# Performance work log

Measured on AMD Instinct MI355X. Metric: run time of the kernel, lower is better.

## Reference

```python
import jax, jax.numpy as jnp
import numpy as np

DIM = 768
HEADS = 12
HEAD_DIM = DIM // HEADS
HIDDEN = 4 * DIM
SCALE = HEAD_DIM ** -0.5
LN_EPS = 1e-5


def layer_norm(x, g, b):
    mu = jnp.mean(x, axis=-1, keepdims=True)
    var = jnp.var(x, axis=-1, keepdims=True)
    return (x - mu) * jax.lax.rsqrt(var + LN_EPS) * g + b


def setup_inputs() -> dict:
    key = jax.random.key(0)
    ks = jax.random.split(key, 10)
    B, N = 2, 2048
    s = 0.02
    return {
        "x": jax.random.normal(ks[0], (B, N, DIM), jnp.float32),
        "elevation": jax.random.uniform(ks[1], (B, N), jnp.float32),
        "qkv_w": jax.random.normal(ks[2], (DIM, 3 * DIM), jnp.float32) * s,
        "qkv_b": jnp.zeros((3 * DIM,), jnp.float32),
        "proj_w": jax.random.normal(ks[3], (DIM, DIM), jnp.float32) * s,
        "proj_b": jnp.zeros((DIM,), jnp.float32),
        "ln1_g": jnp.ones((DIM,), jnp.float32),
        "ln1_b": jnp.zeros((DIM,), jnp.float32),
        "ln2_g": jnp.ones((DIM,), jnp.float32),
        "ln2_b": jnp.zeros((DIM,), jnp.float32),
        "fc1_w": jax.random.normal(ks[4], (DIM, HIDDEN), jnp.float32) * s,
        "fc1_b": jnp.zeros((HIDDEN,), jnp.float32),
        "fc2_w": jax.random.normal(ks[5], (HIDDEN, DIM), jnp.float32) * s,
        "fc2_b": jnp.zeros((DIM,), jnp.float32),
        "barrier": jnp.asarray(3.0, jnp.float32),
    }


def reference(x, elevation, qkv_w, qkv_b, proj_w, proj_b, ln1_g, ln1_b,
              ln2_g, ln2_b, fc1_w, fc1_b, fc2_w, fc2_b, barrier):
    B, N, C = x.shape
    h = layer_norm(x, ln1_g, ln1_b)
    qkv = (h @ qkv_w + qkv_b).reshape(B, N, 3, HEADS, HEAD_DIM)
    q, k, v = jnp.moveaxis(qkv, 2, 0)  # each [B, N, H, D]
    # scores: [B, H, N, N]
    scores = jnp.einsum('bnhd,bmhd->bhnm', q, k) * SCALE
    w = jax.nn.softmax(scores, axis=-1)
    # pairwise elevation mask [B, N, N]: sigmoid(-s * (elev_j - elev_i))
    diff = elevation[:, None, :] - elevation[:, :, None]
    mask = jnp.clip(jax.nn.sigmoid(-barrier * diff), 1e-6, 1.0)
    w = w * mask[:, None, :, :]
    w = w / (jnp.sum(w, axis=-1, keepdims=True) + 1e-8)
    attn_out = jnp.einsum('bhnm,bmhd->bnhd', w, v).reshape(B, N, C)
    x = x + attn_out @ proj_w + proj_b
    h2 = layer_norm(x, ln2_g, ln2_b)
    mlp = jax.nn.gelu(h2 @ fc1_w + fc1_b, approximate=False) @ fc2_w + fc2_b
    return x + mlp
```

## Files before the change

kernel.cpp:

```cpp
#include <hip/hip_runtime.h>
#include <math.h>

#define DIM 768
#define HEADS 12
#define SEQ 2048
#define ROWS 4096
#define LN_EPS 1e-5f

typedef __attribute__((ext_vector_type(8))) short short8;
typedef __attribute__((ext_vector_type(4))) float floatx4;
typedef unsigned short ushort_t;

__device__ __forceinline__ ushort_t f2bf(float x) {
    unsigned u = __float_as_uint(x);
    u += 0x7fff + ((u >> 16) & 1);
    return (ushort_t)(u >> 16);
}

__device__ __forceinline__ void gload_lds16(const void* g, void* l) {
    __builtin_amdgcn_global_load_lds((const __attribute__((address_space(1))) void*)g,
                                     (__attribute__((address_space(3))) void*)l, 16, 0, 0);
}

__launch_bounds__(256)
__global__ void wconv_kernel(const float* __restrict__ W, ushort_t* __restrict__ WT,
                             int K, int N) {
    __shared__ __align__(16) ushort_t s[64][72];
    int k0 = blockIdx.y * 64, n0 = blockIdx.x * 64;
    int t = threadIdx.x;
    int rr0 = t >> 4, c4 = (t & 15) * 4;
    for (int rr = rr0; rr < 64; rr += 16) {
        float4 w = *(const float4*)(W + (size_t)(k0 + rr) * N + n0 + c4);
        s[c4 + 0][rr] = f2bf(w.x); s[c4 + 1][rr] = f2bf(w.y);
        s[c4 + 2][rr] = f2bf(w.z); s[c4 + 3][rr] = f2bf(w.w);
    }
    __syncthreads();
    int nl = t >> 2, kq = (t & 3) * 16;
    uint4 a = *(const uint4*)&s[nl][kq];
    uint4 b = *(const uint4*)&s[nl][kq + 8];
    *(uint4*)(WT + (size_t)(n0 + nl) * K + k0 + kq) = a;
    *(uint4*)(WT + (size_t)(n0 + nl) * K + k0 + kq + 8) = b;
}

__launch_bounds__(256)
__global__ void gelev_kernel(const float* __restrict__ elev, const float* __restrict__ barrier_p,
                             float* __restrict__ G, float* __restrict__ iG,
                             float* __restrict__ C2) {
    int i = blockIdx.x * 256 + threadIdx.x;
    float be = barrier_p[0] * elev[i];
    G[i]  = __expf(be);
    iG[i] = __expf(-be);
    C2[i] = be;
}

__launch_bounds__(256)
__global__ void ln_kernel(const float* __restrict__ x, const float* __restrict__ g,
                          const float* __restrict__ b, ushort_t* __restrict__ out) {
    int row = blockIdx.x;
    const float* xr = x + (size_t)row * DIM;
    int t = threadIdx.x;
    float v0 = xr[t], v1 = xr[t + 256], v2 = xr[t + 512];
    float s  = v0 + v1 + v2;
    float ss = v0 * v0 + v1 * v1 + v2 * v2;
    #pragma unroll
    for (int o = 32; o >= 1; o >>= 1) { s += __shfl_xor(s, o); ss += __shfl_xor(ss, o); }
    __shared__ float rs[4], rss[4];
    int wid = t >> 6, lane = t & 63;
    if (lane == 0) { rs[wid] = s; rss[wid] = ss; }
    __syncthreads();
    if (t == 0) {
        float S = 0.f, SS = 0.f;
        for (int i = 0; i < 4; i++) { S += rs[i]; SS += rss[i]; }
        rs[0] = S; rss[0] = SS;
    }
    __syncthreads();
    float mean = rs[0] * (1.0f / DIM);
    float var  = rss[0] * (1.0f / DIM) - mean * mean;
    float rstd = rsqrtf(var + LN_EPS);
    ushort_t* orow = out + (size_t)row * DIM;
    orow[t]       = f2bf((v0 - mean) * rstd * g[t]       + b[t]);
    orow[t + 256] = f2bf((v1 - mean) * rstd * g[t + 256] + b[t + 256]);
    orow[t + 512] = f2bf((v2 - mean) * rstd * g[t + 512] + b[t + 512]);
}

template<int BN, int EPI>
__launch_bounds__(256)
__global__ void gemm_bf16(const ushort_t* __restrict__ A, const ushort_t* __restrict__ WT,
                          const float* __restrict__ bias, const float* __restrict__ res,
                          float* __restrict__ outF, ushort_t* __restrict__ outB,
                          ushort_t* __restrict__ qb, ushort_t* __restrict__ kb,
                          ushort_t* __restrict__ vb, int N, int K) {
    constexpr int NT = BN / 32;
    __shared__ __align__(16) ushort_t sA[64 * 32];
    __shared__ __align__(16) ushort_t sB[BN * 32];
    int t = threadIdx.x;
    int row0 = blockIdx.y * 64, col0 = blockIdx.x * BN;
    int wid = t >> 6, lane = t & 63;
    int wm = wid >> 1, wn = wid & 1;
    int cl = lane & 15, quad = lane >> 4;

    floatx4 acc[2][NT];
    #pragma unroll
    for (int i = 0; i < 2; i++)
        #pragma unroll
        for (int j = 0; j < NT; j++) { floatx4 z = {0.f, 0.f, 0.f, 0.f}; acc[i][j] = z; }

    for (int k0 = 0; k0 < K; k0 += 32) {
        {
            int r = t >> 2, sub = t & 3;
            gload_lds16(A + (size_t)(row0 + r) * K + k0 + sub * 8, &sA[t * 8]);
        }
        #pragma unroll
        for (int i = 0; i < BN / 64; i++) {
            int c = i * 256 + t;
            int r = c >> 2, sub = c & 3;
            gload_lds16(WT + (size_t)(col0 + r) * K + k0 + sub * 8, &sB[c * 8]);
        }
        __syncthreads();
        short8 a[2], b[NT];
        #pragma unroll
        for (int i = 0; i < 2; i++)
            a[i] = *(const short8*)&sA[(wm * 32 + i * 16 + cl) * 32 + quad * 8];
        #pragma unroll
        for (int j = 0; j < NT; j++)
            b[j] = *(const short8*)&sB[(wn * (BN / 2) + j * 16 + cl) * 32 + quad * 8];
        #pragma unroll
        for (int i = 0; i < 2; i++)
            #pragma unroll
            for (int j = 0; j < NT; j++)
                acc[i][j] = __builtin_amdgcn_mfma_f32_16x16x32_bf16(a[i], b[j], acc[i][j], 0, 0, 0);
        __syncthreads();
    }

    #pragma unroll
    for (int i = 0; i < 2; i++) {
        #pragma unroll
        for (int j = 0; j < NT; j++) {
            int gcol = col0 + wn * (BN / 2) + j * 16 + cl;
            float bv = bias[gcol];
            #pragma unroll
            for (int rg = 0; rg < 4; rg++) {
                int grow = row0 + wm * 32 + i * 16 + quad * 4 + rg;
                float v = acc[i][j][rg] + bv;
                if (EPI == 0) {
                    int which = gcol / 768;
                    int hc = gcol - which * 768;
                    int h = hc >> 6, d = hc & 63;
                    int b_ = grow >> 11, n = grow & 2047;
                    size_t bh = (size_t)(b_ * 12 + h);
                    if (which == 0)      qb[(bh * 2048 + n) * 64 + d] = f2bf(v * 0.125f);
                    else if (which == 1) kb[(bh * 2048 + n) * 64 + d] = f2bf(v);
                    else                 vb[(bh * 64 + d) * 2048 + n] = f2bf(v);
                } else if (EPI == 1) {
                    v = 0.5f * v * (1.f + erff(v * 0.70710678118654752f));
                    outB[(size_t)grow * N + gcol] = f2bf(v);
                } else {
                    v += res[(size_t)grow * N + gcol];
                    outF[(size_t)grow * N + gcol] = v;
                }
            }
        }
    }
}

__launch_bounds__(256)
__global__ void attn_mfma(const ushort_t* __restrict__ qb, const ushort_t* __restrict__ kb,
                          const ushort_t* __restrict__ vb, const float* __restrict__ G,
                          const float* __restrict__ iG, const float* __restrict__ C2,
                          ushort_t* __restrict__ attn) {
    __shared__ __align__(16) ushort_t Qs[64 * 64];
    __shared__ __align__(16) ushort_t Ks[2][64 * 64];
    __shared__ __align__(16) ushort_t Vt[2][64 * 64];
    __shared__ __align__(16) ushort_t Ps[64 * 64];
    __shared__ float Gjs[2][64];
    int qt = blockIdx.x, h = blockIdx.y, b = blockIdx.z;
    int t = threadIdx.x, wid = t >> 6, lane = t & 63;
    int cl = lane & 15, quad = lane >> 4;
    int q0 = qt * 64;
    size_t bh = (size_t)(b * 12 + h);

    const ushort_t* qbase = qb + (bh * 2048 + q0) * 64;
    #pragma unroll
    for (int i = 0; i < 2; i++) {
        int c = i * 256 + t, row = c >> 3, blk = c & 7;
        gload_lds16(qbase + (row << 6) + ((blk ^ (row & 7)) << 3), &Qs[c * 8]);
    }
    int qrow = b * 2048 + q0 + wid * 16 + quad * 4;
    float4 g4  = *(const float4*)(G  + qrow);
    float4 ig4 = *(const float4*)(iG + qrow);
    float4 c24 = *(const float4*)(C2 + qrow);
    float gi[4]  = {g4.x, g4.y, g4.z, g4.w};
    float igi[4] = {ig4.x, ig4.y, ig4.z, ig4.w};
    floatx4 c2init = {c24.x, c24.y, c24.z, c24.w};

    {
        const ushort_t* kbase = kb + bh * 2048 * 64;
        const ushort_t* vbase = vb + bh * 131072;
        #pragma unroll
        for (int i = 0; i < 2; i++) {
            int c = i * 256 + t, row = c >> 3, blk = c & 7;
            gload_lds16(kbase + (row << 6) + ((blk ^ (row & 7)) << 3), &Ks[0][c * 8]);
            gload_lds16(vbase + (size_t)row * 2048 + ((blk ^ (row & 7)) << 3), &Vt[0][c * 8]);
        }
        if (t < 64) Gjs[0][t] = G[b * 2048 + t];
    }

    floatx4 o[4];
    #pragma unroll
    for (int j = 0; j < 4; j++) { floatx4 z = {0.f, 0.f, 0.f, 0.f}; o[j] = z; }
    float se[4] = {0.f, 0.f, 0.f, 0.f}, sem[4] = {0.f, 0.f, 0.f, 0.f};

    for (int kt = 0; kt < 32; kt++) {
        int cur = kt & 1;
        __syncthreads();
        if (kt < 31) {
            int k0n = (kt + 1) * 64;
            const ushort_t* kbase = kb + (bh * 2048 + k0n) * 64;
            const ushort_t* vbase = vb + bh * 131072 + k0n;
            #pragma unroll
            for (int i = 0; i < 2; i++) {
                int c = i * 256 + t, row = c >> 3, blk = c & 7;
                gload_lds16(kbase + (row << 6) + ((blk ^ (row & 7)) << 3), &Ks[cur ^ 1][c * 8]);
                gload_lds16(vbase + (size_t)row * 2048 + ((blk ^ (row & 7)) << 3), &Vt[cur ^ 1][c * 8]);
            }
            if (t < 64) Gjs[cur ^ 1][t] = G[b * 2048 + k0n + t];
        }

        float gjv[4];
        #pragma unroll
        for (int nt = 0; nt < 4; nt++) gjv[nt] = Gjs[cur][nt * 16 + cl];

        floatx4 s[4];
        #pragma unroll
        for (int nt = 0; nt < 4; nt++) s[nt] = c2init;
        #pragma unroll
        for (int kh = 0; kh < 2; kh++) {
            short8 aq = *(const short8*)&Qs[((wid * 16 + cl) << 6) + (((kh * 4 + quad) ^ (cl & 7)) << 3)];
            #pragma unroll
            for (int nt = 0; nt < 4; nt++) {
                short8 bk = *(const short8*)&Ks[cur][((nt * 16 + cl) << 6) + (((kh * 4 + quad) ^ (cl & 7)) << 3)];
                s[nt] = __builtin_amdgcn_mfma_f32_16x16x32_bf16(aq, bk, s[nt], 0, 0, 0);
            }
        }

        #pragma unroll
        for (int rg = 0; rg < 4; rg++) {
            int prow = wid * 16 + quad * 4 + rg;
            int r8 = prow & 7, pbase = prow << 6, csub = cl & 7, chi = cl >> 3;
            #pragma unroll
            for (int nt = 0; nt < 4; nt++) {
                float tf = __expf(s[nt][rg]);
                float R  = __builtin_amdgcn_rcpf(gi[rg] + gjv[nt]);
                float p  = tf * R;
                se[rg]  += tf;
                sem[rg] += p;
                Ps[pbase + (((nt * 2 + chi) ^ r8) << 3) + csub] = (ushort_t)(__float_as_uint(p) >> 16);
            }
        }

        #pragma unroll
        for (int kh = 0; kh < 2; kh++) {
            short8 ap = *(const short8*)&Ps[((wid * 16 + cl) << 6) + (((kh * 4 + quad) ^ (cl & 7)) << 3)];
            #pragma unroll
            for (int dt = 0; dt < 4; dt++) {
                short8 bv = *(const short8*)&Vt[cur][((dt * 16 + cl) << 6) + (((kh * 4 + quad) ^ (cl & 7)) << 3)];
                o[dt] = __builtin_amdgcn_mfma_f32_16x16x32_bf16(ap, bv, o[dt], 0, 0, 0);
            }
        }
    }

    #pragma unroll
    for (int rg = 0; rg < 4; rg++) {
        float a = se[rg], m = sem[rg];
        #pragma unroll
        for (int off = 1; off < 16; off <<= 1) { a += __shfl_xor(a, off); m += __shfl_xor(m, off); }
        float inv = __builtin_amdgcn_rcpf(m + 1e-8f * a * igi[rg]);
        int grow = b * 2048 + q0 + wid * 16 + quad * 4 + rg;
        #pragma unroll
        for (int dt = 0; dt < 4; dt++)
            attn[(size_t)grow * 768 + h * 64 + dt * 16 + cl] = f2bf(o[dt][rg] * inv);
    }
}

extern "C" void kernel_launch(void* const* d_in, const int* in_sizes, int n_in,
                              void* d_out, int out_size, void* d_ws, size_t ws_size,
                              hipStream_t stream) {
    const float* x      = (const float*)d_in[0];
    const float* elev   = (const float*)d_in[1];
    const float* qkv_w  = (const float*)d_in[2];
    const float* qkv_b  = (const float*)d_in[3];
    const float* proj_w = (const float*)d_in[4];
    const float* proj_b = (const float*)d_in[5];
    const float* ln1_g  = (const float*)d_in[6];
    const float* ln1_b  = (const float*)d_in[7];
    const float* ln2_g  = (const float*)d_in[8];
    const float* ln2_b  = (const float*)d_in[9];
    const float* fc1_w  = (const float*)d_in[10];
    const float* fc1_b  = (const float*)d_in[11];
    const float* fc2_w  = (const float*)d_in[12];
    const float* fc2_b  = (const float*)d_in[13];
    const float* barrier= (const float*)d_in[14];
    float* out = (float*)d_out;
    char* ws = (char*)d_ws;

    ushort_t* h    = (ushort_t*)(ws + 0);
    ushort_t* qb   = (ushort_t*)(ws + 6291456);
    ushort_t* kb   = (ushort_t*)(ws + 12582912);
    ushort_t* vb   = (ushort_t*)(ws + 18874368);
    ushort_t* f1   = (ushort_t*)(ws + 0);
    ushort_t* attn = (ushort_t*)(ws + 25165824);
    ushort_t* h2   = (ushort_t*)(ws + 31457280);
    float*    Gf   = (float*)(ws + 31457280);
    float*    iGf  = (float*)(ws + 31473664);
    float*    C2f  = (float*)(ws + 31490048);
    ushort_t* qkvT = (ushort_t*)(ws + 37748736);
    ushort_t* projT= (ushort_t*)(ws + 41287680);
    ushort_t* fc1T = (ushort_t*)(ws + 42467328);
    ushort_t* fc2T = (ushort_t*)(ws + 47185920);

    wconv_kernel<<<dim3(2304 / 64, 768 / 64),  256, 0, stream>>>(qkv_w, qkvT, 768, 2304);
    wconv_kernel<<<dim3(768 / 64,  768 / 64),  256, 0, stream>>>(proj_w, projT, 768, 768);
    wconv_kernel<<<dim3(3072 / 64, 768 / 64),  256, 0, stream>>>(fc1_w, fc1T, 768, 3072);
    wconv_kernel<<<dim3(768 / 64,  3072 / 64), 256, 0, stream>>>(fc2_w, fc2T, 3072, 768);
    gelev_kernel<<<16, 256, 0, stream>>>(elev, barrier, Gf, iGf, C2f);

    ln_kernel<<<ROWS, 256, 0, stream>>>(x, ln1_g, ln1_b, h);
    gemm_bf16<128, 0><<<dim3(2304 / 128, 64), 256, 0, stream>>>(
        h, qkvT, qkv_b, nullptr, nullptr, nullptr, qb, kb, vb, 2304, 768);
    attn_mfma<<<dim3(32, HEADS, 2), 256, 0, stream>>>(qb, kb, vb, Gf, iGf, C2f, attn);
    gemm_bf16<64, 2><<<dim3(768 / 64, 64), 256, 0, stream>>>(
        attn, projT, proj_b, x, out, nullptr, nullptr, nullptr, nullptr, 768, 768);
    ln_kernel<<<ROWS, 256, 0, stream>>>(out, ln2_g, ln2_b, h2);
    gemm_bf16<128, 1><<<dim3(3072 / 128, 64), 256, 0, stream>>>(
        h2, fc1T, fc1_b, nullptr, nullptr, f1, nullptr, nullptr, nullptr, 3072, 768);
    gemm_bf16<64, 2><<<dim3(768 / 64, 64), 256, 0, stream>>>(
        f1, fc2T, fc2_b, out, out, nullptr, nullptr, nullptr, nullptr, 768, 3072);
}
```

Before: 352.9 us.

## Switch attention and QKV/FC1 GEMMs to 32x32 MFMA tiles, merge weight conversions

Adds a 128x128-tile GEMM built on 32x32x16 bf16 MFMA for the QKV and FC1 projections. The attention kernel is rewritten the same way: each wave computes a 32x32 score tile, and the two key-half partial outputs are combined through LDS. Output rows are then staged in LDS and written with coalesced 16-byte stores. The four weight conversion launches are merged into one kernel, and the iG array and the 1e-8 epsilon term in the normaliser are dropped. The aim is fewer MFMA instructions per flop, more data reuse and less launch overhead, at the cost of more registers per thread and an extra LDS reduction and barriers in attention.

```diff
diff --git a/kernel.cpp b/kernel.cpp
--- a/kernel.cpp
+++ b/kernel.cpp
@@ -9,6 +9,7 @@
 
 typedef __attribute__((ext_vector_type(8))) short short8;
 typedef __attribute__((ext_vector_type(4))) float floatx4;
+typedef __attribute__((ext_vector_type(16))) float floatx16;
 typedef unsigned short ushort_t;
 
 __device__ __forceinline__ ushort_t f2bf(float x) {
@@ -23,10 +24,19 @@
 }
 
 __launch_bounds__(256)
-__global__ void wconv_kernel(const float* __restrict__ W, ushort_t* __restrict__ WT,
-                             int K, int N) {
+__global__ void wconv_all(const float* __restrict__ w0, const float* __restrict__ w1,
+                          const float* __restrict__ w2, const float* __restrict__ w3,
+                          ushort_t* __restrict__ t0, ushort_t* __restrict__ t1,
+                          ushort_t* __restrict__ t2, ushort_t* __restrict__ t3) {
     __shared__ __align__(16) ushort_t s[64][72];
-    int k0 = blockIdx.y * 64, n0 = blockIdx.x * 64;
+    int bid = blockIdx.x;
+    const float* W; ushort_t* WT; int K, N, nx, id;
+    if (bid < 432)       { W = w0; WT = t0; K = 768;  N = 2304; nx = 36; id = bid; }
+    else if (bid < 576)  { W = w1; WT = t1; K = 768;  N = 768;  nx = 12; id = bid - 432; }
+    else if (bid < 1152) { W = w2; WT = t2; K = 768;  N = 3072; nx = 48; id = bid - 576; }
+    else                 { W = w3; WT = t3; K = 3072; N = 768;  nx = 12; id = bid - 1152; }
+    int tx = id % nx, ty = id / nx;
+    int k0 = ty * 64, n0 = tx * 64;
     int t = threadIdx.x;
     int rr0 = t >> 4, c4 = (t & 15) * 4;
     for (int rr = rr0; rr < 64; rr += 16) {
@@ -44,12 +54,10 @@
 
 __launch_bounds__(256)
 __global__ void gelev_kernel(const float* __restrict__ elev, const float* __restrict__ barrier_p,
-                             float* __restrict__ G, float* __restrict__ iG,
-                             float* __restrict__ C2) {
+                             float* __restrict__ G, float* __restrict__ C2) {
     int i = blockIdx.x * 256 + threadIdx.x;
     float be = barrier_p[0] * elev[i];
     G[i]  = __expf(be);
-    iG[i] = __expf(-be);
     C2[i] = be;
 }
 
@@ -83,13 +91,91 @@
     orow[t + 512] = f2bf((v2 - mean) * rstd * g[t + 512] + b[t + 512]);
 }
 
+template<int EPI>
+__launch_bounds__(256)
+__global__ void gemm32(const ushort_t* __restrict__ A, const ushort_t* __restrict__ WT,
+                       const float* __restrict__ bias, ushort_t* __restrict__ outB,
+                       ushort_t* __restrict__ qb, ushort_t* __restrict__ kb,
+                       ushort_t* __restrict__ vb, int N, int K) {
+    __shared__ __align__(16) ushort_t sA[128 * 32];
+    __shared__ __align__(16) ushort_t sB[128 * 32];
+    int t = threadIdx.x;
+    int row0 = blockIdx.y * 128, col0 = blockIdx.x * 128;
+    int wid = t >> 6, lane = t & 63, l31 = lane & 31, hb = lane >> 5;
+    int wm = wid >> 1, wn = wid & 1;
+
+    floatx16 acc[2][2];
+    #pragma unroll
+    for (int i = 0; i < 2; i++)
+        #pragma unroll
+        for (int j = 0; j < 2; j++)
+            #pragma unroll
+            for (int e = 0; e < 16; e++) acc[i][j][e] = 0.f;
+
+    for (int k0 = 0; k0 < K; k0 += 32) {
+        #pragma unroll
+        for (int i = 0; i < 2; i++) {
+            int c = i * 256 + t;
+            int r = c >> 2, blk = c & 3;
+            gload_lds16(A  + (size_t)(row0 + r) * K + k0 + ((blk ^ (r & 3)) << 3), &sA[c * 8]);
+            gload_lds16(WT + (size_t)(col0 + r) * K + k0 + ((blk ^ (r & 3)) << 3), &sB[c * 8]);
+        }
+        __syncthreads();
+        #pragma unroll
+        for (int s = 0; s < 2; s++) {
+            int blk = s * 2 + hb;
+            int ra0 = wm * 64 + l31, ra1 = ra0 + 32;
+            int rb0 = wn * 64 + l31, rb1 = rb0 + 32;
+            short8 a0 = *(const short8*)&sA[ra0 * 32 + ((blk ^ (ra0 & 3)) << 3)];
+            short8 a1 = *(const short8*)&sA[ra1 * 32 + ((blk ^ (ra1 & 3)) << 3)];
+            short8 b0 = *(const short8*)&sB[rb0 * 32 + ((blk ^ (rb0 & 3)) << 3)];
+            short8 b1 = *(const short8*)&sB[rb1 * 32 + ((blk ^ (rb1 & 3)) << 3)];
+            acc[0][0] = __builtin_amdgcn_mfma_f32_32x32x16_bf16(a0, b0, acc[0][0], 0, 0, 0);
+            acc[0][1] = __builtin_amdgcn_mfma_f32_32x32x16_bf16(a0, b1, acc[0][1], 0, 0, 0);
+            acc[1][0] = __builtin_amdgcn_mfma_f32_32x32x16_bf16(a1, b0, acc[1][0], 0, 0, 0);
+            acc[1][1] = __builtin_amdgcn_mfma_f32_32x32x16_bf16(a1, b1, acc[1][1], 0, 0, 0);
+        }
+        __syncthreads();
+    }
+
+    #pragma unroll
+    for (int mt = 0; mt < 2; mt++) {
+        #pragma unroll
+        for (int nt = 0; nt < 2; nt++) {
+            int gcol = col0 + wn * 64 + nt * 32 + l31;
+            float bv = bias[gcol];
+            if (EPI == 0) {
+                int which = gcol / 768;
+                int hc = gcol - which * 768;
+                int hh = hc >> 6, d = hc & 63;
+                #pragma unroll
+                for (int rg = 0; rg < 16; rg++) {
+                    int grow = row0 + wm * 64 + mt * 32 + (rg & 3) + 8 * (rg >> 2) + 4 * hb;
+                    float v = acc[mt][nt][rg] + bv;
+                    int b_ = grow >> 11, n = grow & 2047;
+                    size_t bhh = (size_t)(b_ * 12 + hh);
+                    if (which == 0)      qb[(bhh * 2048 + n) * 64 + d] = f2bf(v * 0.125f);
+                    else if (which == 1) kb[(bhh * 2048 + n) * 64 + d] = f2bf(v);
+                    else                 vb[(bhh * 64 + d) * 2048 + n] = f2bf(v);
+                }
+            } else {
+                #pragma unroll
+                for (int rg = 0; rg < 16; rg++) {
+                    int grow = row0 + wm * 64 + mt * 32 + (rg & 3) + 8 * (rg >> 2) + 4 * hb;
+                    float v = acc[mt][nt][rg] + bv;
+                    v = 0.5f * v * (1.f + erff(v * 0.70710678118654752f));
+                    outB[(size_t)grow * N + gcol] = f2bf(v);
+                }
+            }
+        }
+    }
+}
+
 template<int BN, int EPI>
 __launch_bounds__(256)
 __global__ void gemm_bf16(const ushort_t* __restrict__ A, const ushort_t* __restrict__ WT,
                           const float* __restrict__ bias, const float* __restrict__ res,
-                          float* __restrict__ outF, ushort_t* __restrict__ outB,
-                          ushort_t* __restrict__ qb, ushort_t* __restrict__ kb,
-                          ushort_t* __restrict__ vb, int N, int K) {
+                          float* __restrict__ outF, int N, int K) {
     constexpr int NT = BN / 32;
     __shared__ __align__(16) ushort_t sA[64 * 32];
     __shared__ __align__(16) ushort_t sB[BN * 32];
@@ -141,23 +227,8 @@
             #pragma unroll
             for (int rg = 0; rg < 4; rg++) {
                 int grow = row0 + wm * 32 + i * 16 + quad * 4 + rg;
-                float v = acc[i][j][rg] + bv;
-                if (EPI == 0) {
-                    int which = gcol / 768;
-                    int hc = gcol - which * 768;
-                    int h = hc >> 6, d = hc & 63;
-                    int b_ = grow >> 11, n = grow & 2047;
-                    size_t bh = (size_t)(b_ * 12 + h);
-                    if (which == 0)      qb[(bh * 2048 + n) * 64 + d] = f2bf(v * 0.125f);
-                    else if (which == 1) kb[(bh * 2048 + n) * 64 + d] = f2bf(v);
-                    else                 vb[(bh * 64 + d) * 2048 + n] = f2bf(v);
-                } else if (EPI == 1) {
-                    v = 0.5f * v * (1.f + erff(v * 0.70710678118654752f));
-                    outB[(size_t)grow * N + gcol] = f2bf(v);
-                } else {
-                    v += res[(size_t)grow * N + gcol];
-                    outF[(size_t)grow * N + gcol] = v;
-                }
+                float v = acc[i][j][rg] + bv + res[(size_t)grow * N + gcol];
+                outF[(size_t)grow * N + gcol] = v;
             }
         }
     }
@@ -166,18 +237,17 @@
 __launch_bounds__(256)
 __global__ void attn_mfma(const ushort_t* __restrict__ qb, const ushort_t* __restrict__ kb,
                           const ushort_t* __restrict__ vb, const float* __restrict__ G,
-                          const float* __restrict__ iG, const float* __restrict__ C2,
-                          ushort_t* __restrict__ attn) {
-    __shared__ __align__(16) ushort_t Qs[64 * 64];
-    __shared__ __align__(16) ushort_t Ks[2][64 * 64];
-    __shared__ __align__(16) ushort_t Vt[2][64 * 64];
-    __shared__ __align__(16) ushort_t Ps[64 * 64];
-    __shared__ float Gjs[2][64];
-    int qt = blockIdx.x, h = blockIdx.y, b = blockIdx.z;
-    int t = threadIdx.x, wid = t >> 6, lane = t & 63;
-    int cl = lane & 15, quad = lane >> 4;
+                          const float* __restrict__ C2, ushort_t* __restrict__ attn) {
+    __shared__ __align__(16) ushort_t Qs[4096];
+    __shared__ __align__(16) ushort_t Ks[2][4096];
+    __shared__ __align__(16) ushort_t Vt[2][4096];
+    __shared__ __align__(16) ushort_t Ps[4096];
+    __shared__ float semL[2][64];
+    int qt = blockIdx.x, hh = blockIdx.y, b = blockIdx.z;
+    int t = threadIdx.x, wid = t >> 6, lane = t & 63, l31 = lane & 31, hb = lane >> 5;
+    int wm = wid >> 1, wn = wid & 1;
     int q0 = qt * 64;
-    size_t bh = (size_t)(b * 12 + h);
+    size_t bh = (size_t)(b * 12 + hh);
 
     const ushort_t* qbase = qb + (bh * 2048 + q0) * 64;
     #pragma unroll
@@ -185,13 +255,14 @@
         int c = i * 256 + t, row = c >> 3, blk = c & 7;
         gload_lds16(qbase + (row << 6) + ((blk ^ (row & 7)) << 3), &Qs[c * 8]);
     }
-    int qrow = b * 2048 + q0 + wid * 16 + quad * 4;
-    float4 g4  = *(const float4*)(G  + qrow);
-    float4 ig4 = *(const float4*)(iG + qrow);
-    float4 c24 = *(const float4*)(C2 + qrow);
-    float gi[4]  = {g4.x, g4.y, g4.z, g4.w};
-    float igi[4] = {ig4.x, ig4.y, ig4.z, ig4.w};
-    floatx4 c2init = {c24.x, c24.y, c24.z, c24.w};
+
+    float gi[16]; floatx16 c2v;
+    #pragma unroll
+    for (int rg = 0; rg < 16; rg++) {
+        int rr = (rg & 3) + 8 * (rg >> 2) + 4 * hb;
+        int gr = b * 2048 + q0 + wm * 32 + rr;
+        gi[rg] = G[gr]; c2v[rg] = C2[gr];
+    }
 
     {
         const ushort_t* kbase = kb + bh * 2048 * 64;
@@ -202,13 +273,14 @@
             gload_lds16(kbase + (row << 6) + ((blk ^ (row & 7)) << 3), &Ks[0][c * 8]);
             gload_lds16(vbase + (size_t)row * 2048 + ((blk ^ (row & 7)) << 3), &Vt[0][c * 8]);
         }
-        if (t < 64) Gjs[0][t] = G[b * 2048 + t];
-    }
-
-    floatx4 o[4];
-    #pragma unroll
-    for (int j = 0; j < 4; j++) { floatx4 z = {0.f, 0.f, 0.f, 0.f}; o[j] = z; }
-    float se[4] = {0.f, 0.f, 0.f, 0.f}, sem[4] = {0.f, 0.f, 0.f, 0.f};
+    }
+
+    floatx16 o0, o1;
+    float semP[16];
+    #pragma unroll
+    for (int e = 0; e < 16; e++) { o0[e] = 0.f; o1[e] = 0.f; semP[e] = 0.f; }
+
+    int arow = wm * 32 + l31, brow = wn * 32 + l31, x7 = l31 & 7;
 
     for (int kt = 0; kt < 32; kt++) {
         int cur = kt & 1;
@@ -223,63 +295,81 @@
                 gload_lds16(kbase + (row << 6) + ((blk ^ (row & 7)) << 3), &Ks[cur ^ 1][c * 8]);
                 gload_lds16(vbase + (size_t)row * 2048 + ((blk ^ (row & 7)) << 3), &Vt[cur ^ 1][c * 8]);
             }
-            if (t < 64) Gjs[cur ^ 1][t] = G[b * 2048 + k0n + t];
-        }
-
-        float gjv[4];
-        #pragma unroll
-        for (int nt = 0; nt < 4; nt++) gjv[nt] = Gjs[cur][nt * 16 + cl];
-
-        floatx4 s[4];
-        #pragma unroll
-        for (int nt = 0; nt < 4; nt++) s[nt] = c2init;
-        #pragma unroll
-        for (int kh = 0; kh < 2; kh++) {
-            short8 aq = *(const short8*)&Qs[((wid * 16 + cl) << 6) + (((kh * 4 + quad) ^ (cl & 7)) << 3)];
-            #pragma unroll
-            for (int nt = 0; nt < 4; nt++) {
-                short8 bk = *(const short8*)&Ks[cur][((nt * 16 + cl) << 6) + (((kh * 4 + quad) ^ (cl & 7)) << 3)];
-                s[nt] = __builtin_amdgcn_mfma_f32_16x16x32_bf16(aq, bk, s[nt], 0, 0, 0);
-            }
-        }
-
-        #pragma unroll
-        for (int rg = 0; rg < 4; rg++) {
-            int prow = wid * 16 + quad * 4 + rg;
-            int r8 = prow & 7, pbase = prow << 6, csub = cl & 7, chi = cl >> 3;
-            #pragma unroll
-            for (int nt = 0; nt < 4; nt++) {
-                float tf = __expf(s[nt][rg]);
-                float R  = __builtin_amdgcn_rcpf(gi[rg] + gjv[nt]);
-                float p  = tf * R;
-                se[rg]  += tf;
-                sem[rg] += p;
-                Ps[pbase + (((nt * 2 + chi) ^ r8) << 3) + csub] = (ushort_t)(__float_as_uint(p) >> 16);
-            }
-        }
-
-        #pragma unroll
-        for (int kh = 0; kh < 2; kh++) {
-            short8 ap = *(const short8*)&Ps[((wid * 16 + cl) << 6) + (((kh * 4 + quad) ^ (cl & 7)) << 3)];
-            #pragma unroll
-            for (int dt = 0; dt < 4; dt++) {
-                short8 bv = *(const short8*)&Vt[cur][((dt * 16 + cl) << 6) + (((kh * 4 + quad) ^ (cl & 7)) << 3)];
-                o[dt] = __builtin_amdgcn_mfma_f32_16x16x32_bf16(ap, bv, o[dt], 0, 0, 0);
-            }
-        }
-    }
-
-    #pragma unroll
-    for (int rg = 0; rg < 4; rg++) {
-        float a = se[rg], m = sem[rg];
-        #pragma unroll
-        for (int off = 1; off < 16; off <<= 1) { a += __shfl_xor(a, off); m += __shfl_xor(m, off); }
-        float inv = __builtin_amdgcn_rcpf(m + 1e-8f * a * igi[rg]);
-        int grow = b * 2048 + q0 + wid * 16 + quad * 4 + rg;
-        #pragma unroll
-        for (int dt = 0; dt < 4; dt++)
-            attn[(size_t)grow * 768 + h * 64 + dt * 16 + cl] = f2bf(o[dt][rg] * inv);
-    }
+        }
+        float gj = G[b * 2048 + kt * 64 + wn * 32 + l31];
+
+        floatx16 s = c2v;
+        #pragma unroll
+        for (int s4 = 0; s4 < 4; s4++) {
+            short8 aq = *(const short8*)&Qs[(arow << 6) + (((s4 * 2 + hb) ^ x7) << 3)];
+            short8 bk = *(const short8*)&Ks[cur][(brow << 6) + (((s4 * 2 + hb) ^ x7) << 3)];
+            s = __builtin_amdgcn_mfma_f32_32x32x16_bf16(aq, bk, s, 0, 0, 0);
+        }
+
+        #pragma unroll
+        for (int rg = 0; rg < 16; rg++) {
+            int rr = (rg & 3) + 8 * (rg >> 2) + 4 * hb;
+            int qrow = wm * 32 + rr;
+            float tf = __expf(s[rg]);
+            float p  = tf * __builtin_amdgcn_rcpf(gi[rg] + gj);
+            semP[rg] += p;
+            Ps[(qrow << 6) + (((wn * 4 + (l31 >> 3)) ^ (qrow & 7)) << 3) + (l31 & 7)] =
+                (ushort_t)(__float_as_uint(p) >> 16);
+        }
+
+        #pragma unroll
+        for (int s2 = 0; s2 < 2; s2++) {
+            int blk = wn * 4 + s2 * 2 + hb;
+            short8 ap  = *(const short8*)&Ps[(arow << 6) + ((blk ^ x7) << 3)];
+            short8 bv0 = *(const short8*)&Vt[cur][(l31 << 6) + ((blk ^ x7) << 3)];
+            short8 bv1 = *(const short8*)&Vt[cur][((32 + l31) << 6) + ((blk ^ x7) << 3)];
+            o0 = __builtin_amdgcn_mfma_f32_32x32x16_bf16(ap, bv0, o0, 0, 0, 0);
+            o1 = __builtin_amdgcn_mfma_f32_32x32x16_bf16(ap, bv1, o1, 0, 0, 0);
+        }
+    }
+
+    #pragma unroll
+    for (int rg = 0; rg < 16; rg++) {
+        float v = semP[rg];
+        v += __shfl_xor(v, 1);  v += __shfl_xor(v, 2);  v += __shfl_xor(v, 4);
+        v += __shfl_xor(v, 8);  v += __shfl_xor(v, 16);
+        semP[rg] = v;
+    }
+    #pragma unroll
+    for (int rg = 0; rg < 16; rg++) {
+        int rr = (rg & 3) + 8 * (rg >> 2) + 4 * hb;
+        if (l31 == rr) semL[wn][wm * 32 + rr] = semP[rg];
+    }
+    __syncthreads();
+    float* oL = (float*)Ks;
+    if (wn == 0) {
+        #pragma unroll
+        for (int rg = 0; rg < 16; rg++) {
+            int rr = (rg & 3) + 8 * (rg >> 2) + 4 * hb;
+            oL[wm * 2048 + (rr << 6) + l31]      = o0[rg];
+            oL[wm * 2048 + (rr << 6) + 32 + l31] = o1[rg];
+        }
+    }
+    __syncthreads();
+    if (wn == 1) {
+        #pragma unroll
+        for (int rg = 0; rg < 16; rg++) {
+            int rr = (rg & 3) + 8 * (rg >> 2) + 4 * hb;
+            int qrow = wm * 32 + rr;
+            float inv = __builtin_amdgcn_rcpf(semL[0][qrow] + semL[1][qrow]);
+            float v0 = o0[rg] + oL[wm * 2048 + (rr << 6) + l31];
+            float v1 = o1[rg] + oL[wm * 2048 + (rr << 6) + 32 + l31];
+            Ps[(qrow << 6) + ((((l31 >> 3)) ^ (qrow & 7)) << 3) + (l31 & 7)]     = f2bf(v0 * inv);
+            Ps[(qrow << 6) + (((4 + (l31 >> 3)) ^ (qrow & 7)) << 3) + (l31 & 7)] = f2bf(v1 * inv);
+        }
+    }
+    __syncthreads();
+    int row = t >> 2, ch = t & 3;
+    uint4 u0 = *(const uint4*)&Ps[(row << 6) + (((ch * 2    ) ^ (row & 7)) << 3)];
+    uint4 u1 = *(const uint4*)&Ps[(row << 6) + (((ch * 2 + 1) ^ (row & 7)) << 3)];
+    size_t oa = (size_t)(b * 2048 + q0 + row) * 768 + hh * 64 + ch * 16;
+    *(uint4*)(attn + oa)     = u0;
+    *(uint4*)(attn + oa + 8) = u1;
 }
 
 extern "C" void kernel_launch(void* const* d_in, const int* in_sizes, int n_in,
@@ -311,28 +401,24 @@
     ushort_t* attn = (ushort_t*)(ws + 25165824);
     ushort_t* h2   = (ushort_t*)(ws + 31457280);
     float*    Gf   = (float*)(ws + 31457280);
-    float*    iGf  = (float*)(ws + 31473664);
-    float*    C2f  = (float*)(ws + 31490048);
+    float*    C2f  = (float*)(ws + 31473664);
     ushort_t* qkvT = (ushort_t*)(ws + 37748736);
     ushort_t* projT= (ushort_t*)(ws + 41287680);
     ushort_t* fc1T = (ushort_t*)(ws + 42467328);
     ushort_t* fc2T = (ushort_t*)(ws + 47185920);
 
-    wconv_kernel<<<dim3(2304 / 64, 768 / 64),  256, 0, stream>>>(qkv_w, qkvT, 768, 2304);
-    wconv_kernel<<<dim3(768 / 64,  768 / 64),  256, 0, stream>>>(proj_w, projT, 768, 768);
-    wconv_kernel<<<dim3(3072 / 64, 768 / 64),  256, 0, stream>>>(fc1_w, fc1T, 768, 3072);
-    wconv_kernel<<<dim3(768 / 64,  3072 / 64), 256, 0, stream>>>(fc2_w, fc2T, 3072, 768);
-    gelev_kernel<<<16, 256, 0, stream>>>(elev, barrier, Gf, iGf, C2f);
+    wconv_all<<<1728, 256, 0, stream>>>(qkv_w, proj_w, fc1_w, fc2_w, qkvT, projT, fc1T, fc2T);
+    gelev_kernel<<<16, 256, 0, stream>>>(elev, barrier, Gf, C2f);
 
     ln_kernel<<<ROWS, 256, 0, stream>>>(x, ln1_g, ln1_b, h);
-    gemm_bf16<128, 0><<<dim3(2304 / 128, 64), 256, 0, stream>>>(
-        h, qkvT, qkv_b, nullptr, nullptr, nullptr, qb, kb, vb, 2304, 768);
-    attn_mfma<<<dim3(32, HEADS, 2), 256, 0, stream>>>(qb, kb, vb, Gf, iGf, C2f, attn);
+    gemm32<0><<<dim3(2304 / 128, 32), 256, 0, stream>>>(
+        h, qkvT, qkv_b, nullptr, qb, kb, vb, 2304, 768);
+    attn_mfma<<<dim3(32, HEADS, 2), 256, 0, stream>>>(qb, kb, vb, Gf, C2f, attn);
     gemm_bf16<64, 2><<<dim3(768 / 64, 64), 256, 0, stream>>>(
-        attn, projT, proj_b, x, out, nullptr, nullptr, nullptr, nullptr, 768, 768);
+        attn, projT, proj_b, x, out, 768, 768);
     ln_kernel<<<ROWS, 256, 0, stream>>>(out, ln2_g, ln2_b, h2);
-    gemm_bf16<128, 1><<<dim3(3072 / 128, 64), 256, 0, stream>>>(
-        h2, fc1T, fc1_b, nullptr, nullptr, f1, nullptr, nullptr, nullptr, 3072, 768);
+    gemm32<1><<<dim3(3072 / 128, 32), 256, 0, stream>>>(
+        h2, fc1T, fc1_b, f1, nullptr, nullptr, nullptr, 3072, 768);
     gemm_bf16<64, 2><<<dim3(768 / 64, 64), 256, 0, stream>>>(
-        f1, fc2T, fc2_b, out, out, nullptr, nullptr, nullptr, nullptr, 768, 3072);
-}
+        f1, fc2T, fc2_b, out, out, 768, 3072);
+}
```

Result: no change. 346.6 us (-1.8%).
